# Performance work log

Hardware: AMD Instinct MI355X
Metric: run time of the kernel (lower is better)

Reference implementation:

```python
import jax, jax.numpy as jnp
import numpy as np

B, CIN, COUT, H, W, KS, PAD = 8, 64, 128, 32, 32, 3, 1
OH, OW = H, W  # stride 1, pad 1, dilation 1 -> same spatial size
QMIN, QMAX = -128, 127


def setup_inputs() -> dict:
    key = jax.random.key(0)
    k1, k2, k3 = jax.random.split(key, 3)
    x = jax.random.normal(k1, (B, CIN, H, W), jnp.float32)
    weight = jax.random.normal(k2, (COUT, CIN, KS, KS), jnp.float32) * 0.05
    bias = jax.random.normal(k3, (COUT,), jnp.float32) * 0.01
    # exact int8 product LUT: lut[a+128, b+128] = a*b (the 'approximate multiplier' table)
    q = jnp.arange(QMIN, QMAX + 1, dtype=jnp.int32)  # [256]
    lut = q[:, None] * q[None, :]                     # [256,256] int32
    # gradient LUT: d(a*b)/da = b, d(a*b)/db = a
    gradient_lut = jnp.stack([
        jnp.broadcast_to(q[None, :], (256, 256)),
        jnp.broadcast_to(q[:, None], (256, 256)),
    ]).astype(jnp.float32)                            # [2,256,256]
    T_feature = jnp.ones((1,), jnp.float32)
    T_weight = jnp.ones((1,), jnp.float32)
    return {"x": x, "weight": weight, "bias": bias, "lut": lut,
            "gradient_lut": gradient_lut, "T_feature": T_feature, "T_weight": T_weight}


def _quantize(v, T):
    scale = 127.0 / T
    return jnp.clip(jnp.round(v * scale), QMIN, QMAX).astype(jnp.int32)


def _lut_conv(xq, wq, lut):
    """LUT-based int8 conv. xq [B,CIN,H,W] int32 in [-128,127], wq [COUT,CIN,KS,KS]."""
    xp = jnp.pad(xq, ((0, 0), (0, 0), (PAD, PAD), (PAD, PAD)))
    # im2col: 9 structurally-distinct kernel offsets (fixed small loop)
    patches = jnp.stack([xp[:, :, i:i + OH, j:j + OW]
                         for i in range(KS) for j in range(KS)], axis=2)  # [B,CIN,9,OH,OW]
    K = CIN * KS * KS
    cols = patches.transpose(0, 3, 4, 1, 2).reshape(B * OH * OW, K)  # [P,K]
    wf = wq.reshape(COUT, K)                                         # [COUT,K]
    lut_flat = lut.reshape(-1)

    def step(acc, xs):
        xk, wk = xs  # xk [P], wk [COUT]
        idx = (xk[:, None] + 128) * 256 + (wk[None, :] + 128)  # [P,COUT]
        return acc + lut_flat[idx], None

    acc0 = jnp.zeros((B * OH * OW, COUT), jnp.int32)
    acc, _ = jax.lax.scan(step, acc0, (cols.T, wf.T))  # scan over K patch elems
    return acc.reshape(B, OH, OW, COUT).transpose(0, 3, 1, 2)  # [B,COUT,OH,OW]


def reference(x, weight, bias, lut, gradient_lut, T_feature, T_weight):
    # EMA threshold update (update_T_func), detached scalars in the original
    Tf = 0.95 * T_feature[0] + 0.05 * jnp.max(jnp.abs(x))
    Tw = 0.95 * T_weight[0] + 0.05 * jnp.max(jnp.abs(weight))
    xq = _quantize(x, Tf)
    wq = _quantize(weight, Tw)
    acc = _lut_conv(xq, wq, lut).astype(jnp.float32)
    out = acc * ((Tf / 127.0) * (Tw / 127.0)) + bias[None, :, None, None]
    return out
```

## Files before the change

kernel.cpp:

```cpp
#include <hip/hip_runtime.h>
#include <cstdint>

#define BATCH 8
#define CIN 64
#define COUT 128
#define HH 32
#define WW 32

typedef int v4i __attribute__((ext_vector_type(4)));
typedef float v4f __attribute__((ext_vector_type(4)));

#define WS_TW 1
#define WS_PX 16
#define WFRAG_OFF 4096

__device__ __forceinline__ unsigned quantb(float v, float scale) {
    float q = rintf(v * scale);
    q = fminf(fmaxf(q, -128.0f), 127.0f);
    return ((unsigned)(int)q) & 255u;
}

__global__ __launch_bounds__(256) void prep(const float* __restrict__ x,
                                            const float* __restrict__ w,
                                            const float* __restrict__ Tw_in,
                                            float* __restrict__ ws_f32,
                                            uint8_t* __restrict__ wfrag) {
    int blk = blockIdx.x;
    int t = threadIdx.x;
    int lane = t & 63;
    int wave = t >> 6;
    __shared__ float sm[4];

    if (blk < 128) {
        const float4* p = (const float4*)x;
        int base = blk * 1024 + t;
        float m = 0.0f;
        #pragma unroll
        for (int k = 0; k < 4; ++k) {
            float4 v = p[base + k * 256];
            m = fmaxf(m, fmaxf(fmaxf(fabsf(v.x), fabsf(v.y)), fmaxf(fabsf(v.z), fabsf(v.w))));
        }
        #pragma unroll
        for (int off = 32; off > 0; off >>= 1)
            m = fmaxf(m, __shfl_xor(m, off, 64));
        if (lane == 0) sm[wave] = m;
        __syncthreads();
        if (t == 0)
            ws_f32[WS_PX + blk] = fmaxf(fmaxf(sm[0], sm[1]), fmaxf(sm[2], sm[3]));
    } else {
        const float4* w4 = (const float4*)w;
        float m = 0.0f;
        #pragma unroll 8
        for (int i = 0; i < 72; ++i) {
            float4 v = w4[t + i * 256];
            m = fmaxf(m, fmaxf(fmaxf(fabsf(v.x), fabsf(v.y)), fmaxf(fabsf(v.z), fabsf(v.w))));
        }
        #pragma unroll
        for (int off = 32; off > 0; off >>= 1)
            m = fmaxf(m, __shfl_xor(m, off, 64));
        if (lane == 0) sm[wave] = m;
        __syncthreads();
        float Mw = fmaxf(fmaxf(sm[0], sm[1]), fmaxf(sm[2], sm[3]));
        float Tw = 0.95f * Tw_in[0] + 0.05f * Mw;
        if (blk == 128 && t == 0) ws_f32[WS_TW] = Tw;
        float scale = 127.0f / Tw;

        int wb = blk - 128;
        #pragma unroll
        for (int k = 0; k < 4; ++k) {
            int d = wb * 1024 + k * 256 + t;
            int idx4 = d * 4;
            int j0 = idx4 & 15;
            int ln = (idx4 >> 4) & 63;
            int f  = idx4 >> 10;
            int g = f & 7;
            int tap = f >> 3;
            int kh = tap / 3, kw = tap - kh * 3;
            int co = g * 16 + (ln & 15);
            int ci0 = (ln >> 4) * 16 + j0;
            unsigned pack = 0;
            #pragma unroll
            for (int c = 0; c < 4; ++c) {
                float v = w[((co * CIN + ci0 + c) * 3 + kh) * 3 + kw];
                pack |= quantb(v, scale) << (8 * c);
            }
            ((unsigned*)wfrag)[d] = pack;
        }
    }
}

__global__ __launch_bounds__(256, 2) void conv_fused(const float* __restrict__ x,
                                                     const uint8_t* __restrict__ wfrag,
                                                     const float* __restrict__ bias,
                                                     const float* __restrict__ Tf_in,
                                                     const float* __restrict__ ws_f32,
                                                     float* __restrict__ out) {
    int blk = blockIdx.x;
    int t = threadIdx.x;
    int lane = t & 63;
    int wave = t >> 6;
    int nb = blk & 1;
    int mb = blk >> 1;
    int b = mb >> 5;
    int oh = mb & 31;

    __shared__ unsigned stg[3 * 64 * 9];
    __shared__ unsigned tile[3 * 34 * 16];

    float mx = fmaxf(ws_f32[WS_PX + lane], ws_f32[WS_PX + 64 + lane]);
    #pragma unroll
    for (int off = 32; off > 0; off >>= 1)
        mx = fmaxf(mx, __shfl_xor(mx, off, 64));
    float Tf = 0.95f * Tf_in[0] + 0.05f * mx;
    float Tw = ws_f32[WS_TW];
    float scale = 127.0f / Tf;

    #pragma unroll
    for (int k = 0; k < 7; ++k) {
        int i = t + k * 256;
        if (i < 3 * 34 * 16) tile[i] = 0u;
    }

    const float4* x4 = (const float4*)x;
    #pragma unroll
    for (int k = 0; k < 6; ++k) {
        int f = t + k * 256;
        int ci = f / 24;
        int rem = f - ci * 24;
        int r = rem >> 3, wq = rem & 7;
        int ih = oh - 1 + r;
        if (ih >= 0 && ih < HH) {
            float4 v = x4[(b * CIN + ci) * 256 + ih * 8 + wq];
            unsigned pack = quantb(v.x, scale) | (quantb(v.y, scale) << 8) |
                            (quantb(v.z, scale) << 16) | (quantb(v.w, scale) << 24);
            stg[(r * 64 + ci) * 9 + wq] = pack;
        }
    }
    __syncthreads();

    const uint8_t* stgb = (const uint8_t*)stg;
    #pragma unroll
    for (int k = 0; k < 6; ++k) {
        int o = t + k * 256;
        int c4 = o & 15;
        int q = o >> 4;
        int ww_ = q & 31;
        int r = q >> 5;
        int ih = oh - 1 + r;
        if (ih >= 0 && ih < HH) {
            unsigned d = (unsigned)stgb[(r * 64 + c4 * 4 + 0) * 36 + ww_]
                       | ((unsigned)stgb[(r * 64 + c4 * 4 + 1) * 36 + ww_] << 8)
                       | ((unsigned)stgb[(r * 64 + c4 * 4 + 2) * 36 + ww_] << 16)
                       | ((unsigned)stgb[(r * 64 + c4 * 4 + 3) * 36 + ww_] << 24);
            tile[(r * 34 + ww_ + 1) * 16 + c4] = d;
        }
    }
    __syncthreads();

    int mt = wave & 1;
    int nh2 = wave >> 1;
    int row = lane & 15;
    int quad = lane >> 4;
    int px0 = mt * 16 + row;

    v4i acc[2];
    acc[0] = (v4i){0, 0, 0, 0};
    acc[1] = (v4i){0, 0, 0, 0};

    const uint8_t* tb = (const uint8_t*)tile;

    #pragma unroll
    for (int tp = 0; tp < 9; ++tp) {
        const int kh = tp / 3, kw = tp % 3;
        v4i afrag = *(const v4i*)(tb + ((kh * 34 + px0 + kw) * 64) + quad * 16);
        #pragma unroll
        for (int nt = 0; nt < 2; ++nt) {
            int g = nb * 4 + nh2 * 2 + nt;
            v4i bfrag = *(const v4i*)(wfrag + (((tp * 8 + g) * 64) + lane) * 16);
            acc[nt] = __builtin_amdgcn_mfma_i32_16x16x64_i8(afrag, bfrag, acc[nt], 0, 0, 0);
        }
    }

    float s = (Tf / 127.0f) * (Tw / 127.0f);
    int ow0 = mt * 16 + quad * 4;
    #pragma unroll
    for (int nt = 0; nt < 2; ++nt) {
        int g = nb * 4 + nh2 * 2 + nt;
        int co = g * 16 + row;
        float bb = bias[co];
        v4f o;
        o.x = (float)acc[nt][0] * s + bb;
        o.y = (float)acc[nt][1] * s + bb;
        o.z = (float)acc[nt][2] * s + bb;
        o.w = (float)acc[nt][3] * s + bb;
        __builtin_nontemporal_store(o, (v4f*)(out + (((b * COUT + co) * HH + oh) * WW) + ow0));
    }
}

extern "C" void kernel_launch(void* const* d_in, const int* in_sizes, int n_in,
                              void* d_out, int out_size, void* d_ws, size_t ws_size,
                              hipStream_t stream) {
    const float* x         = (const float*)d_in[0];
    const float* weight    = (const float*)d_in[1];
    const float* bias      = (const float*)d_in[2];
    const float* T_feature = (const float*)d_in[5];
    const float* T_weight  = (const float*)d_in[6];

    float*   ws_f32 = (float*)d_ws;
    uint8_t* wfrag  = (uint8_t*)d_ws + WFRAG_OFF;

    prep<<<146, 256, 0, stream>>>(x, weight, T_weight, ws_f32, wfrag);
    conv_fused<<<512, 256, 0, stream>>>(x, wfrag, bias, T_feature, ws_f32,
                                        (float*)d_out);
}
```

Baseline: 86.54 us.

## Transpose input tile in registers with byte permutes and pad LDS pitch

Each thread now loads four channel rows of the input, quantizes them, and transposes the 4x4 byte block in registers with v_perm before writing straight into the LDS tile. This removes the intermediate staging buffer, one barrier and the byte-wise LDS gathers. The tile pitch is padded from 16 to 18 words to cut bank conflicts, which means the A-fragment reads become two 8-byte loads instead of one 16-byte load. Zeroing now covers only the halo columns and the out-of-range rows, the prep block order is swapped so the weight blocks launch first, and the weight max loop gets four independent accumulators.

```diff
diff --git a/kernel.cpp b/kernel.cpp
--- a/kernel.cpp
+++ b/kernel.cpp
@@ -13,6 +13,8 @@
 #define WS_TW 1
 #define WS_PX 16
 #define WFRAG_OFF 4096
+
+#define TPITCH 18
 
 __device__ __forceinline__ unsigned quantb(float v, float scale) {
     float q = rintf(v * scale);
@@ -31,9 +33,10 @@
     int wave = t >> 6;
     __shared__ float sm[4];
 
-    if (blk < 128) {
+    if (blk >= 18) {
         const float4* p = (const float4*)x;
-        int base = blk * 1024 + t;
+        int xb = blk - 18;
+        int base = xb * 1024 + t;
         float m = 0.0f;
         #pragma unroll
         for (int k = 0; k < 4; ++k) {
@@ -46,15 +49,22 @@
         if (lane == 0) sm[wave] = m;
         __syncthreads();
         if (t == 0)
-            ws_f32[WS_PX + blk] = fmaxf(fmaxf(sm[0], sm[1]), fmaxf(sm[2], sm[3]));
+            ws_f32[WS_PX + xb] = fmaxf(fmaxf(sm[0], sm[1]), fmaxf(sm[2], sm[3]));
     } else {
         const float4* w4 = (const float4*)w;
-        float m = 0.0f;
-        #pragma unroll 8
-        for (int i = 0; i < 72; ++i) {
-            float4 v = w4[t + i * 256];
-            m = fmaxf(m, fmaxf(fmaxf(fabsf(v.x), fabsf(v.y)), fmaxf(fabsf(v.z), fabsf(v.w))));
-        }
+        float m0 = 0.0f, m1 = 0.0f, m2 = 0.0f, m3 = 0.0f;
+        #pragma unroll
+        for (int i = 0; i < 72; i += 4) {
+            float4 a = w4[t + (i + 0) * 256];
+            float4 bv = w4[t + (i + 1) * 256];
+            float4 c = w4[t + (i + 2) * 256];
+            float4 d = w4[t + (i + 3) * 256];
+            m0 = fmaxf(m0, fmaxf(fmaxf(fabsf(a.x), fabsf(a.y)), fmaxf(fabsf(a.z), fabsf(a.w))));
+            m1 = fmaxf(m1, fmaxf(fmaxf(fabsf(bv.x), fabsf(bv.y)), fmaxf(fabsf(bv.z), fabsf(bv.w))));
+            m2 = fmaxf(m2, fmaxf(fmaxf(fabsf(c.x), fabsf(c.y)), fmaxf(fabsf(c.z), fabsf(c.w))));
+            m3 = fmaxf(m3, fmaxf(fmaxf(fabsf(d.x), fabsf(d.y)), fmaxf(fabsf(d.z), fabsf(d.w))));
+        }
+        float m = fmaxf(fmaxf(m0, m1), fmaxf(m2, m3));
         #pragma unroll
         for (int off = 32; off > 0; off >>= 1)
             m = fmaxf(m, __shfl_xor(m, off, 64));
@@ -62,10 +72,10 @@
         __syncthreads();
         float Mw = fmaxf(fmaxf(sm[0], sm[1]), fmaxf(sm[2], sm[3]));
         float Tw = 0.95f * Tw_in[0] + 0.05f * Mw;
-        if (blk == 128 && t == 0) ws_f32[WS_TW] = Tw;
+        if (blk == 0 && t == 0) ws_f32[WS_TW] = Tw;
         float scale = 127.0f / Tw;
 
-        int wb = blk - 128;
+        int wb = blk;
         #pragma unroll
         for (int k = 0; k < 4; ++k) {
             int d = wb * 1024 + k * 256 + t;
@@ -104,55 +114,76 @@
     int b = mb >> 5;
     int oh = mb & 31;
 
-    __shared__ unsigned stg[3 * 64 * 9];
-    __shared__ unsigned tile[3 * 34 * 16];
-
-    float mx = fmaxf(ws_f32[WS_PX + lane], ws_f32[WS_PX + 64 + lane]);
+    __shared__ unsigned tile[3 * 34 * TPITCH];
+
+    float p0 = ws_f32[WS_PX + lane];
+    float p1 = ws_f32[WS_PX + 64 + lane];
+    float Tw = ws_f32[WS_TW];
+
+    if (t < 96) {
+        int rr = t >> 5;
+        int rest = t & 31;
+        int side = rest >> 4;
+        int kk = rest & 15;
+        tile[(rr * 34 + side * 33) * TPITCH + kk] = 0u;
+    }
+    if (oh == 0 || oh == 31) {
+        int rbad = (oh == 0) ? 0 : 2;
+        #pragma unroll
+        for (int k = 0; k < 3; ++k) {
+            int i = t + k * 256;
+            if (i < 544) {
+                int px = i >> 4, kk = i & 15;
+                tile[(rbad * 34 + px) * TPITCH + kk] = 0u;
+            }
+        }
+    }
+
+    float mx = fmaxf(p0, p1);
     #pragma unroll
     for (int off = 32; off > 0; off >>= 1)
         mx = fmaxf(mx, __shfl_xor(mx, off, 64));
     float Tf = 0.95f * Tf_in[0] + 0.05f * mx;
-    float Tw = ws_f32[WS_TW];
     float scale = 127.0f / Tf;
 
-    #pragma unroll
-    for (int k = 0; k < 7; ++k) {
-        int i = t + k * 256;
-        if (i < 3 * 34 * 16) tile[i] = 0u;
-    }
-
     const float4* x4 = (const float4*)x;
     #pragma unroll
-    for (int k = 0; k < 6; ++k) {
-        int f = t + k * 256;
-        int ci = f / 24;
-        int rem = f - ci * 24;
-        int r = rem >> 3, wq = rem & 7;
-        int ih = oh - 1 + r;
-        if (ih >= 0 && ih < HH) {
-            float4 v = x4[(b * CIN + ci) * 256 + ih * 8 + wq];
-            unsigned pack = quantb(v.x, scale) | (quantb(v.y, scale) << 8) |
-                            (quantb(v.z, scale) << 16) | (quantb(v.w, scale) << 24);
-            stg[(r * 64 + ci) * 9 + wq] = pack;
-        }
-    }
-    __syncthreads();
-
-    const uint8_t* stgb = (const uint8_t*)stg;
-    #pragma unroll
-    for (int k = 0; k < 6; ++k) {
-        int o = t + k * 256;
-        int c4 = o & 15;
-        int q = o >> 4;
-        int ww_ = q & 31;
-        int r = q >> 5;
-        int ih = oh - 1 + r;
-        if (ih >= 0 && ih < HH) {
-            unsigned d = (unsigned)stgb[(r * 64 + c4 * 4 + 0) * 36 + ww_]
-                       | ((unsigned)stgb[(r * 64 + c4 * 4 + 1) * 36 + ww_] << 8)
-                       | ((unsigned)stgb[(r * 64 + c4 * 4 + 2) * 36 + ww_] << 16)
-                       | ((unsigned)stgb[(r * 64 + c4 * 4 + 3) * 36 + ww_] << 24);
-            tile[(r * 34 + ww_ + 1) * 16 + c4] = d;
+    for (int k = 0; k < 2; ++k) {
+        int j = t + k * 256;
+        if (j < 384) {
+            int r = j >> 7;
+            int rem = j & 127;
+            int wq = rem >> 4;
+            int g4 = rem & 15;
+            int ih = oh - 1 + r;
+            if (ih >= 0 && ih < HH) {
+                int xb = (b * CIN + g4 * 4) * 256 + ih * 8 + wq;
+                float4 v0 = x4[xb];
+                float4 v1 = x4[xb + 256];
+                float4 v2 = x4[xb + 512];
+                float4 v3 = x4[xb + 768];
+                unsigned P0 = quantb(v0.x, scale) | (quantb(v0.y, scale) << 8) |
+                              (quantb(v0.z, scale) << 16) | (quantb(v0.w, scale) << 24);
+                unsigned P1 = quantb(v1.x, scale) | (quantb(v1.y, scale) << 8) |
+                              (quantb(v1.z, scale) << 16) | (quantb(v1.w, scale) << 24);
+                unsigned P2 = quantb(v2.x, scale) | (quantb(v2.y, scale) << 8) |
+                              (quantb(v2.z, scale) << 16) | (quantb(v2.w, scale) << 24);
+                unsigned P3 = quantb(v3.x, scale) | (quantb(v3.y, scale) << 8) |
+                              (quantb(v3.z, scale) << 16) | (quantb(v3.w, scale) << 24);
+                unsigned Q0 = __builtin_amdgcn_perm(P1, P0, 0x05040100u);
+                unsigned Q1 = __builtin_amdgcn_perm(P1, P0, 0x07060302u);
+                unsigned Q2 = __builtin_amdgcn_perm(P3, P2, 0x05040100u);
+                unsigned Q3 = __builtin_amdgcn_perm(P3, P2, 0x07060302u);
+                unsigned D0 = __builtin_amdgcn_perm(Q2, Q0, 0x06040200u);
+                unsigned D1 = __builtin_amdgcn_perm(Q2, Q0, 0x07050301u);
+                unsigned D2 = __builtin_amdgcn_perm(Q3, Q1, 0x06040200u);
+                unsigned D3 = __builtin_amdgcn_perm(Q3, Q1, 0x07050301u);
+                int base = (r * 34 + wq * 4 + 1) * TPITCH + g4;
+                tile[base]              = D0;
+                tile[base + TPITCH]     = D1;
+                tile[base + 2 * TPITCH] = D2;
+                tile[base + 3 * TPITCH] = D3;
+            }
         }
     }
     __syncthreads();
@@ -167,12 +198,15 @@
     acc[0] = (v4i){0, 0, 0, 0};
     acc[1] = (v4i){0, 0, 0, 0};
 
-    const uint8_t* tb = (const uint8_t*)tile;
+    const int2* tl2 = (const int2*)tile;
 
     #pragma unroll
     for (int tp = 0; tp < 9; ++tp) {
         const int kh = tp / 3, kw = tp % 3;
-        v4i afrag = *(const v4i*)(tb + ((kh * 34 + px0 + kw) * 64) + quad * 16);
+        int d = ((kh * 34) + px0 + kw) * TPITCH + quad * 4;
+        int2 lo = tl2[(d >> 1)];
+        int2 hi = tl2[(d >> 1) + 1];
+        v4i afrag = (v4i){lo.x, lo.y, hi.x, hi.y};
         #pragma unroll
         for (int nt = 0; nt < 2; ++nt) {
             int g = nb * 4 + nh2 * 2 + nt;
```

After: 78.51 us. 1.1x faster.
